# Performance work log

Measured on AMD Instinct MI355X. Metric: run time of the kernel, lower is better.

## Reference

```python
import jax, jax.numpy as jnp
import numpy as np

N = 100000  # nodes
E = 1600000  # edges (before self-loops)
F_IN, F_HID, F_OUT = 64, 128, 64


def setup_inputs() -> dict:
    key = jax.random.key(0)
    ks = jax.random.split(key, 8)
    x = jax.random.normal(ks[0], (N, F_IN), dtype=jnp.float32)
    edge_index = jax.random.randint(ks[1], (2, E), 0, N, dtype=jnp.int64)
    # Glorot-ish init for weights, zero bias (PyG GCNConv default)
    W1 = jax.random.normal(ks[2], (F_IN, F_HID), dtype=jnp.float32) / np.sqrt(F_IN)
    W2 = jax.random.normal(ks[3], (F_HID, F_HID), dtype=jnp.float32) / np.sqrt(F_HID)
    W3 = jax.random.normal(ks[4], (F_HID, F_OUT), dtype=jnp.float32) / np.sqrt(F_HID)
    b1 = jnp.zeros((F_HID,), dtype=jnp.float32)
    b2 = jnp.zeros((F_HID,), dtype=jnp.float32)
    b3 = jnp.zeros((F_OUT,), dtype=jnp.float32)
    return {"x": x, "edge_index": edge_index, "W1": W1, "b1": b1,
            "W2": W2, "b2": b2, "W3": W3, "b3": b3}


def _gcn_norm(edge_index, num_nodes):
    """Add self-loops and compute symmetric D^-1/2 A D^-1/2 edge norms."""
    loop = jnp.arange(num_nodes, dtype=edge_index.dtype)
    src = jnp.concatenate([edge_index[0], loop])  # [E+N]
    dst = jnp.concatenate([edge_index[1], loop])  # [E+N]
    deg = jax.ops.segment_sum(jnp.ones_like(src, dtype=jnp.float32), dst,
                              num_segments=num_nodes)
    dinv = jnp.where(deg > 0, jax.lax.rsqrt(deg), 0.0)
    norm = dinv[src] * dinv[dst]  # [E+N]
    return src, dst, norm


def _gcn_conv(h, src, dst, norm, W, b, num_nodes):
    hw = h @ W                                   # [N, out] dense transform
    msg = hw[src] * norm[:, None]                # gather + edge scale
    out = jax.ops.segment_sum(msg, dst, num_segments=num_nodes)  # scatter-add
    return out + b


def reference(x, edge_index, W1, b1, W2, b2, W3, b3):
    src, dst, norm = _gcn_norm(edge_index, N)
    h = jax.nn.relu(_gcn_conv(x, src, dst, norm, W1, b1, N))
    h = jax.nn.relu(_gcn_conv(h, src, dst, norm, W2, b2, N))
    return _gcn_conv(h, src, dst, norm, W3, b3, N)
```

## Files before the change

### kernel.cpp

```cpp
#include <hip/hip_runtime.h>
#include <hip/hip_bf16.h>
#include <hip/hip_fp16.h>


typedef _Float16 h8 __attribute__((ext_vector_type(8)));
typedef float f4 __attribute__((ext_vector_type(4)));

constexpr int BSHIFT = 7;
constexpr int BNODES = 1 << BSHIFT;
constexpr int PB     = 256;
constexpr int CAP    = 4096;

__device__ inline void load8h(const _Float16* p, float* f) {
    h8 v = *(const h8*)p;
#pragma unroll
    for (int j = 0; j < 8; j++) f[j] = (float)v[j];
}

__device__ inline void store8h(_Float16* p, const float* f) {
    h8 v;
#pragma unroll
    for (int j = 0; j < 8; j++) v[j] = (_Float16)f[j];
    *(h8*)p = v;
}

__device__ inline void store4h(_Float16* p, float4 v) {
    _Float16 t[4] = {(_Float16)v.x, (_Float16)v.y, (_Float16)v.z, (_Float16)v.w};
    *(uint2*)p = *(uint2*)t;
}

__global__ __launch_bounds__(256) void phist_k(const int* __restrict__ dst,
                                               int* __restrict__ hist,
                                               int E, int nbuck, int chunk) {
    __shared__ int h[1024];
    for (int i = threadIdx.x; i < nbuck; i += 256) h[i] = 0;
    __syncthreads();
    int beg = blockIdx.x * chunk;
    int end = min(E, beg + chunk);
    for (int e = beg + threadIdx.x; e < end; e += 256)
        atomicAdd(&h[dst[e] >> BSHIFT], 1);
    __syncthreads();
    for (int i = threadIdx.x; i < nbuck; i += 256)
        hist[(long)blockIdx.x * nbuck + i] = h[i];
}

__global__ __launch_bounds__(256) void scan_blocks_k(const int* __restrict__ in,
                                                     int* __restrict__ excl,
                                                     int* __restrict__ bsums, int n) {
    __shared__ int s[256];
    int tid = threadIdx.x;
    int i = blockIdx.x * 256 + tid;
    int v = (i < n) ? in[i] : 0;
    s[tid] = v;
    __syncthreads();
    for (int off = 1; off < 256; off <<= 1) {
        int t = (tid >= off) ? s[tid - off] : 0;
        __syncthreads();
        s[tid] += t;
        __syncthreads();
    }
    if (i < n) excl[i] = s[tid] - v;
    if (tid == 255) bsums[blockIdx.x] = s[255];
}

__global__ __launch_bounds__(1024) void mid_k(int* __restrict__ bsums, int nb,
                                              const int* __restrict__ hist,
                                              int* __restrict__ bbase,
                                              int nbuck, int E) {
    __shared__ int s[1024];
    int tid = threadIdx.x;
    int v = 0;
    if (blockIdx.x == 0) {
        v = (tid < nb) ? bsums[tid] : 0;
    } else {
        if (tid < nbuck) {
            int t0 = 0, t1 = 0, t2 = 0, t3 = 0;
            for (int j = 0; j < PB; j += 4) {
                t0 += hist[(long)(j + 0) * nbuck + tid];
                t1 += hist[(long)(j + 1) * nbuck + tid];
                t2 += hist[(long)(j + 2) * nbuck + tid];
                t3 += hist[(long)(j + 3) * nbuck + tid];
            }
            v = (t0 + t1) + (t2 + t3);
        }
    }
    s[tid] = v;
    __syncthreads();
    for (int off = 1; off < 1024; off <<= 1) {
        int t = (tid >= off) ? s[tid - off] : 0;
        __syncthreads();
        s[tid] += t;
        __syncthreads();
    }
    if (blockIdx.x == 0) {
        if (tid < nb) bsums[tid] = s[tid] - v;
    } else {
        if (tid < nbuck) bbase[tid] = s[tid] - v;
        if (tid == 0) bbase[nbuck] = E;
    }
}

__global__ __launch_bounds__(256) void part2_k(const int* __restrict__ src,
                                               const int* __restrict__ dst,
                                               const int* __restrict__ offs,
                                               const int* __restrict__ bsums,
                                               unsigned* __restrict__ ebuf,
                                               int E, int nbuck, int chunk) {
    __shared__ int cur[1024];
    for (int i = threadIdx.x; i < nbuck; i += 256) {
        long flat = (long)blockIdx.x * nbuck + i;
        cur[i] = offs[flat] + bsums[flat >> 8];
    }
    __syncthreads();
    int beg = blockIdx.x * chunk;
    int end = min(E, beg + chunk);
    for (int e = beg + threadIdx.x; e < end; e += 256) {
        int d = dst[e];
        int b = d >> BSHIFT;
        int pos = atomicAdd(&cur[b], 1);
        ebuf[pos] = ((unsigned)(d & (BNODES - 1)) << 25) | (unsigned)src[e];
    }
}

__global__ __launch_bounds__(256) void finalize_k(const unsigned* __restrict__ ebuf,
                                                  const int* __restrict__ hist,
                                                  const int* __restrict__ offs,
                                                  const int* __restrict__ bsums,
                                                  const int* __restrict__ bbase,
                                                  int nbuck,
                                                  int* __restrict__ rowst,
                                                  int* __restrict__ rowend,
                                                  float* __restrict__ dinv,
                                                  int* __restrict__ col,
                                                  const float* __restrict__ x,
                                                  _Float16* __restrict__ msgX, int N) {
    __shared__ unsigned se[CAP];
    __shared__ int cj[PB], sj[PB], sb[PB];
    __shared__ int cnt_s[BNODES], scan_s[BNODES], cur_s[BNODES];
    __shared__ float di_s[BNODES];

    int b = blockIdx.x, tid = threadIdx.x;
    int node0 = b << BSHIFT;
    int nn = min(BNODES, N - node0);
    int beg = bbase[b];

    if (tid < PB) {
        long flat = (long)tid * nbuck + b;
        cj[tid] = hist[flat];
        sj[tid] = offs[flat] + bsums[flat >> 8];
    }
    if (tid < BNODES) cnt_s[tid] = 0;
    __syncthreads();

    if (tid < PB) sb[tid] = cj[tid];
    __syncthreads();
    for (int off = 1; off < PB; off <<= 1) {
        int t = 0;
        if (tid < PB && tid >= off) t = sb[tid - off];
        __syncthreads();
        if (tid < PB) sb[tid] += t;
        __syncthreads();
    }
    int m = sb[PB - 1];
    __syncthreads();

    {
        int j = tid;
        int base = sb[j] - cj[j], c = cj[j], s0 = sj[j];
        for (int k = 0; k < c; k++) {
            unsigned e = ebuf[s0 + k];
            int idx = base + k;
            if (idx < CAP) se[idx] = e;
            else atomicAdd(&cnt_s[e >> 25], 1);
        }
    }
    __syncthreads();

    int mcap = m < CAP ? m : CAP;
    for (int i = tid; i < mcap; i += 256) atomicAdd(&cnt_s[se[i] >> 25], 1);
    __syncthreads();

    int v = (tid < BNODES) ? cnt_s[tid] : 0;
    if (tid < BNODES) scan_s[tid] = v;
    __syncthreads();
    for (int off = 1; off < BNODES; off <<= 1) {
        int t = 0;
        if (tid < BNODES && tid >= off) t = scan_s[tid - off];
        __syncthreads();
        if (tid < BNODES) scan_s[tid] += t;
        __syncthreads();
    }
    if (tid < nn) {
        int ex = scan_s[tid] - v;
        int st = beg + ex;
        rowst[node0 + tid] = st;
        rowend[node0 + tid] = st + v;
        float di = rsqrtf((float)v + 1.0f);
        dinv[node0 + tid] = di;
        di_s[tid] = di;
        cur_s[tid] = ex;
    }
    __syncthreads();

    for (int i = tid; i < mcap; i += 256) {
        unsigned e = se[i];
        int p = atomicAdd(&cur_s[e >> 25], 1);
        col[beg + p] = (int)(e & 0x1FFFFFFu);
    }
    if (m > CAP) {
        int j = tid;
        int base = sb[j] - cj[j], c = cj[j], s0 = sj[j];
        for (int k = 0; k < c; k++) {
            int idx = base + k;
            if (idx >= CAP) {
                unsigned e = ebuf[s0 + k];
                int p = atomicAdd(&cur_s[e >> 25], 1);
                col[beg + p] = (int)(e & 0x1FFFFFFu);
            }
        }
    }

    for (int t = tid; t < nn * 16; t += 256) {
        int nl = t >> 4, q = t & 15;
        int node = node0 + nl;
        float4 vx = *(const float4*)(x + (long)node * 64 + q * 4);
        float di = di_s[nl];
        vx.x *= di; vx.y *= di; vx.z *= di; vx.w *= di;
        store4h(msgX + (long)node * 64 + q * 4, vx);
    }
}

template <int K, int FOUT, bool BIAS, bool RELU, bool DINV_OUT, bool SMOUT>
__global__ __launch_bounds__(256) void fag_k(const _Float16* __restrict__ msg,
                                             const int* __restrict__ rowst,
                                             const int* __restrict__ rowend,
                                             const int* __restrict__ col,
                                             const float* __restrict__ dinv,
                                             const _Float16* __restrict__ Wsw,
                                             const float* __restrict__ bias,
                                             _Float16* __restrict__ C, int n) {
    constexpr int NT = FOUT / 16, NC = K / 32;
    constexpr int LDK = K + 8;
    constexpr int LPN = K / 8;
    constexpr int NPB = 256 / LPN;
    __shared__ _Float16 As[64 * LDK];

    int tid = threadIdx.x;
    int row0 = blockIdx.x * 64;

#pragma unroll
    for (int pass = 0; pass < 64 / NPB; pass++) {
        int nl = pass * NPB + tid / LPN;
        int q = tid % LPN;
        int node = row0 + nl;
        float acc[8];
        if (node < n) {
            load8h(msg + (long)node * K + q * 8, acc);
            int beg = rowst[node], end = rowend[node];
            int e = beg;
            for (; e + 4 <= end; e += 4) {
                int s0 = col[e], s1 = col[e + 1], s2 = col[e + 2], s3 = col[e + 3];
                h8 v0 = *(const h8*)(msg + (long)s0 * K + q * 8);
                h8 v1 = *(const h8*)(msg + (long)s1 * K + q * 8);
                h8 v2 = *(const h8*)(msg + (long)s2 * K + q * 8);
                h8 v3 = *(const h8*)(msg + (long)s3 * K + q * 8);
#pragma unroll
                for (int j = 0; j < 8; j++)
                    acc[j] += ((float)v0[j] + (float)v1[j]) + ((float)v2[j] + (float)v3[j]);
            }
            for (; e < end; e++) {
                int s = col[e];
                h8 v = *(const h8*)(msg + (long)s * K + q * 8);
#pragma unroll
                for (int j = 0; j < 8; j++) acc[j] += (float)v[j];
            }
            float di = dinv[node];
#pragma unroll
            for (int j = 0; j < 8; j++) acc[j] *= di;
        } else {
#pragma unroll
            for (int j = 0; j < 8; j++) acc[j] = 0.f;
        }
        h8 o;
#pragma unroll
        for (int j = 0; j < 8; j++) o[j] = (_Float16)acc[j];
        *(h8*)(As + nl * LDK + q * 8) = o;
    }
    __syncthreads();

    int lane = tid & 63, wave = tid >> 6;
    int quad = lane >> 4, cl = lane & 15;
    int r0 = wave * 16;

    h8 a[NC];
#pragma unroll
    for (int c = 0; c < NC; c++)
        a[c] = *(const h8*)(As + (r0 + cl) * LDK + quad * 8 + c * 32);

    f4 acc2[NT];
#pragma unroll
    for (int t = 0; t < NT; t++) acc2[t] = (f4){0.f, 0.f, 0.f, 0.f};

    const h8* wv = (const h8*)Wsw;
#pragma unroll
    for (int c = 0; c < NC; c++) {
#pragma unroll
        for (int t = 0; t < NT; t++)
            acc2[t] = __builtin_amdgcn_mfma_f32_16x16x32_f16(
                a[c], wv[(c * NT + t) * 64 + lane], acc2[t], 0, 0, 0);
    }

#pragma unroll
    for (int t = 0; t < NT; t++) {
        int c0 = t * 16 + cl;
        float bb = BIAS ? bias[c0] : 0.f;
#pragma unroll
        for (int r = 0; r < 4; r++) {
            int row = row0 + r0 + quad * 4 + r;
            if (row >= n) continue;
            float v = acc2[t][r] + bb;
            if (RELU) v = fmaxf(v, 0.f);
            if (DINV_OUT) v *= dinv[row];
            if (SMOUT)
                C[((long)t * n + row) * 16 + cl] = (_Float16)v;
            else
                C[(long)row * FOUT + c0] = (_Float16)v;
        }
    }
}

__global__ __launch_bounds__(256) void agg_sm2_k(const _Float16* __restrict__ msg,
                                                 const int* __restrict__ rowst,
                                                 const int* __restrict__ rowend,
                                                 const int* __restrict__ col,
                                                 const float* __restrict__ dinv,
                                                 _Float16* __restrict__ out, int n) {
    int slice = blockIdx.x & 7;
    int blk   = blockIdx.x >> 3;
    int node  = blk * 128 + (threadIdx.x >> 1);
    int q     = threadIdx.x & 1;
    if (node >= n) return;
    const _Float16* mp = msg + (long)slice * n * 16 + q * 8;

    float acc[8];
    load8h(mp + (long)node * 16, acc);

    int beg = rowst[node], end = rowend[node];
    int e = beg;
    for (; e + 8 <= end; e += 8) {
        h8 v[8];
#pragma unroll
        for (int u = 0; u < 8; u++)
            v[u] = *(const h8*)(mp + (long)col[e + u] * 16);
#pragma unroll
        for (int j = 0; j < 8; j++)
            acc[j] += (((float)v[0][j] + (float)v[1][j]) + ((float)v[2][j] + (float)v[3][j])) +
                      (((float)v[4][j] + (float)v[5][j]) + ((float)v[6][j] + (float)v[7][j]));
    }
    for (; e + 4 <= end; e += 4) {
        h8 v0 = *(const h8*)(mp + (long)col[e] * 16);
        h8 v1 = *(const h8*)(mp + (long)col[e + 1] * 16);
        h8 v2 = *(const h8*)(mp + (long)col[e + 2] * 16);
        h8 v3 = *(const h8*)(mp + (long)col[e + 3] * 16);
#pragma unroll
        for (int j = 0; j < 8; j++)
            acc[j] += ((float)v0[j] + (float)v1[j]) + ((float)v2[j] + (float)v3[j]);
    }
    for (; e < end; e++) {
        h8 v = *(const h8*)(mp + (long)col[e] * 16);
#pragma unroll
        for (int j = 0; j < 8; j++) acc[j] += (float)v[j];
    }

    float di = dinv[node];
    float o[8];
#pragma unroll
    for (int j = 0; j < 8; j++) o[j] = di * acc[j];
    store8h(out + (long)node * 128 + slice * 16 + q * 8, o);
}

__global__ __launch_bounds__(256) void agg_sm3_k(const _Float16* __restrict__ msg,
                                                 const int* __restrict__ rowst,
                                                 const int* __restrict__ rowend,
                                                 const int* __restrict__ col,
                                                 const float* __restrict__ dinv,
                                                 const float* __restrict__ b,
                                                 float* __restrict__ out, int n) {
    int slice = blockIdx.x & 7;
    int blk   = blockIdx.x >> 3;
    int node  = blk * 256 + threadIdx.x;
    if (node >= n) return;
    const _Float16* mp = msg + (long)slice * n * 8;

    float acc[8];
    load8h(mp + (long)node * 8, acc);

    int beg = rowst[node], end = rowend[node];
    int e = beg;
    for (; e + 8 <= end; e += 8) {
        h8 v[8];
#pragma unroll
        for (int u = 0; u < 8; u++)
            v[u] = *(const h8*)(mp + (long)col[e + u] * 8);
#pragma unroll
        for (int j = 0; j < 8; j++)
            acc[j] += (((float)v[0][j] + (float)v[1][j]) + ((float)v[2][j] + (float)v[3][j])) +
                      (((float)v[4][j] + (float)v[5][j]) + ((float)v[6][j] + (float)v[7][j]));
    }
    for (; e + 4 <= end; e += 4) {
        h8 v0 = *(const h8*)(mp + (long)col[e] * 8);
        h8 v1 = *(const h8*)(mp + (long)col[e + 1] * 8);
        h8 v2 = *(const h8*)(mp + (long)col[e + 2] * 8);
        h8 v3 = *(const h8*)(mp + (long)col[e + 3] * 8);
#pragma unroll
        for (int j = 0; j < 8; j++)
            acc[j] += ((float)v0[j] + (float)v1[j]) + ((float)v2[j] + (float)v3[j]);
    }
    for (; e < end; e++) {
        h8 v = *(const h8*)(mp + (long)col[e] * 8);
#pragma unroll
        for (int j = 0; j < 8; j++) acc[j] += (float)v[j];
    }

    float di = dinv[node];
    float o[8];
#pragma unroll
    for (int j = 0; j < 8; j++) o[j] = di * acc[j] + b[slice * 8 + j];
    float* d = out + (long)node * 64 + slice * 8;
    *(float4*)d = make_float4(o[0], o[1], o[2], o[3]);
    *(float4*)(d + 4) = make_float4(o[4], o[5], o[6], o[7]);
}

template <int K, int FOUT>
__device__ inline void wfrag(const float* __restrict__ W,
                             _Float16* __restrict__ Wsw, int t) {
    constexpr int NT = FOUT / 16;
    int lane = t & 63;
    int tile = (t >> 6) % NT;
    int chunk = (t >> 6) / NT;
    int kbase = chunk * 32 + (lane >> 4) * 8;
    int nc = tile * 16 + (lane & 15);
    h8 v;
#pragma unroll
    for (int j = 0; j < 8; j++) v[j] = (_Float16)W[(kbase + j) * FOUT + nc];
    ((h8*)Wsw)[t] = v;
}

__global__ __launch_bounds__(256) void wprep3_k(const float* __restrict__ W1,
                                                const float* __restrict__ W2,
                                                const float* __restrict__ W3,
                                                _Float16* __restrict__ w1s,
                                                _Float16* __restrict__ w2s,
                                                _Float16* __restrict__ w3s) {
    int t = blockIdx.x * 256 + threadIdx.x;
    if (t < 1024) wfrag<64, 128>(W1, w1s, t);
    else if (t < 3072) wfrag<128, 128>(W2, w2s, t - 1024);
    else if (t < 4096) wfrag<128, 64>(W3, w3s, t - 3072);
}

__global__ __launch_bounds__(256) void dgemm_k(const _Float16* __restrict__ A,
                                               const _Float16* __restrict__ w2s,
                                               const _Float16* __restrict__ w3s,
                                               const float* __restrict__ b2,
                                               const float* __restrict__ dinv,
                                               _Float16* __restrict__ C, int n) {
    constexpr int LDK = 136;
    __shared__ _Float16 Hs[64 * LDK];

    int tid = threadIdx.x, lane = tid & 63, wave = tid >> 6;
    int quad = lane >> 4, cl = lane & 15;
    int row0 = blockIdx.x * 64, r0 = wave * 16;

    h8 a[4];
    const _Float16* arow = A + (long)(row0 + r0 + cl) * 128 + quad * 8;
#pragma unroll
    for (int c = 0; c < 4; c++) a[c] = *(const h8*)(arow + c * 32);

    f4 acc1[8];
#pragma unroll
    for (int t = 0; t < 8; t++) acc1[t] = (f4){0.f, 0.f, 0.f, 0.f};
    const h8* wv2 = (const h8*)w2s;
#pragma unroll
    for (int c = 0; c < 4; c++) {
#pragma unroll
        for (int t = 0; t < 8; t++)
            acc1[t] = __builtin_amdgcn_mfma_f32_16x16x32_f16(
                a[c], wv2[(c * 8 + t) * 64 + lane], acc1[t], 0, 0, 0);
    }

#pragma unroll
    for (int t = 0; t < 8; t++) {
        int c0 = t * 16 + cl;
        float bb = b2[c0];
#pragma unroll
        for (int r = 0; r < 4; r++) {
            float v = fmaxf(acc1[t][r] + bb, 0.f);
            Hs[(r0 + quad * 4 + r) * LDK + c0] = (_Float16)v;
        }
    }
    __builtin_amdgcn_s_waitcnt(0);

    h8 a2[4];
#pragma unroll
    for (int c = 0; c < 4; c++)
        a2[c] = *(const h8*)(Hs + (r0 + cl) * LDK + quad * 8 + c * 32);

    f4 acc2[4];
#pragma unroll
    for (int t = 0; t < 4; t++) acc2[t] = (f4){0.f, 0.f, 0.f, 0.f};
    const h8* wv3 = (const h8*)w3s;
#pragma unroll
    for (int c = 0; c < 4; c++) {
#pragma unroll
        for (int t = 0; t < 4; t++)
            acc2[t] = __builtin_amdgcn_mfma_f32_16x16x32_f16(
                a2[c], wv3[(c * 4 + t) * 64 + lane], acc2[t], 0, 0, 0);
    }

#pragma unroll
    for (int t = 0; t < 4; t++) {
        int c0 = t * 16 + cl;
        int sl = c0 >> 3, sp = c0 & 7;
#pragma unroll
        for (int r = 0; r < 4; r++) {
            int row = row0 + r0 + quad * 4 + r;
            if (row >= n) continue;
            float v = acc2[t][r] * dinv[row];
            C[((long)sl * n + row) * 8 + sp] = (_Float16)v;
        }
    }
}

extern "C" void kernel_launch(void* const* d_in, const int* in_sizes, int n_in,
                              void* d_out, int out_size, void* d_ws, size_t ws_size,
                              hipStream_t stream) {
    const float* x  = (const float*)d_in[0];
    const int*   ei = (const int*)d_in[1];
    const float* W1 = (const float*)d_in[2];
    const float* b1 = (const float*)d_in[3];
    const float* W2 = (const float*)d_in[4];
    const float* b2 = (const float*)d_in[5];
    const float* W3 = (const float*)d_in[6];
    const float* b3 = (const float*)d_in[7];
    float* out = (float*)d_out;

    const int N = in_sizes[0] / 64;
    const int E = in_sizes[1] / 2;
    const int* src = ei;
    const int* dst = ei + E;
    const int nbuck = (N + BNODES - 1) >> BSHIFT;
    const int chunk = (E + PB - 1) / PB;
    const int n2 = PB * nbuck;
    const int nb2 = (n2 + 255) / 256;

    int*   hist   = (int*)d_ws;
    int*   offs   = hist + n2;
    int*   bsums  = offs + n2;
    int*   bbase  = bsums + 1024;
    int*   rowst  = bbase + nbuck + 1;
    int*   rowend = rowst + N;
    float* dinv   = (float*)(rowend + N);
    int*   col    = (int*)(dinv + N);
    _Float16* w1s = (_Float16*)(col + E);
    _Float16* w2s = w1s + 64 * 128;
    _Float16* w3s = w2s + 128 * 128;
    float* P      = (float*)(w3s + 128 * 64);
    float* Q      = P + (long)N * 128;

    _Float16* msgX  = (_Float16*)P;
    unsigned* ebuf  = (unsigned*)Q;
    _Float16* msg1  = (_Float16*)Q;
    _Float16* aggH1 = (_Float16*)P;
    _Float16* msg3  = (_Float16*)Q;

    const int gb = (N + 63) / 64;

    wprep3_k<<<16, 256, 0, stream>>>(W1, W2, W3, w1s, w2s, w3s);

    phist_k<<<PB, 256, 0, stream>>>(dst, hist, E, nbuck, chunk);
    scan_blocks_k<<<nb2, 256, 0, stream>>>(hist, offs, bsums, n2);
    mid_k<<<2, 1024, 0, stream>>>(bsums, nb2, hist, bbase, nbuck, E);
    part2_k<<<PB, 256, 0, stream>>>(src, dst, offs, bsums, ebuf, E, nbuck, chunk);
    finalize_k<<<nbuck, 256, 0, stream>>>(ebuf, hist, offs, bsums, bbase, nbuck,
                                          rowst, rowend, dinv, col, x, msgX, N);

    fag_k<64, 128, true, true, true, true><<<gb, 256, 0, stream>>>(
        msgX, rowst, rowend, col, dinv, w1s, b1, msg1, N);

    const int nb128 = (N + 127) / 128;
    agg_sm2_k<<<8 * nb128, 256, 0, stream>>>(
        msg1, rowst, rowend, col, dinv, aggH1, N);

    dgemm_k<<<gb, 256, 0, stream>>>(aggH1, w2s, w3s, b2, dinv, msg3, N);

    const int nb256 = (N + 255) / 256;
    agg_sm3_k<<<8 * nb256, 256, 0, stream>>>(
        msg3, rowst, rowend, col, dinv, b3, out, N);
}
```

Measured before the change: 433.3 us.

## Split each node's edge list across 8 lanes with shuffle reduction in aggregation

Both aggregation kernels now give each node 8 threads, which take edges in an interleaved stride and combine partial sums with xor-shuffles, instead of one or two threads walking the whole edge list. The layer-2 aggregation output is also written slice-major, and the dense GEMM reads its A operand from that layout so each store is contiguous. The aim is more memory-level parallelism per node and less load imbalance from skewed degrees. The cost is more threads per node, shuffle overhead, and a loss of long per-thread unrolled gather chains.

```diff
diff --git a/kernel.cpp b/kernel.cpp
--- a/kernel.cpp
+++ b/kernel.cpp
@@ -329,7 +329,7 @@
     }
 }
 
-__global__ __launch_bounds__(256) void agg_sm2_k(const _Float16* __restrict__ msg,
+__global__ __launch_bounds__(256) void agg_ep2_k(const _Float16* __restrict__ msg,
                                                  const int* __restrict__ rowst,
                                                  const int* __restrict__ rowend,
                                                  const int* __restrict__ col,
@@ -337,49 +337,53 @@
                                                  _Float16* __restrict__ out, int n) {
     int slice = blockIdx.x & 7;
     int blk   = blockIdx.x >> 3;
-    int node  = blk * 128 + (threadIdx.x >> 1);
-    int q     = threadIdx.x & 1;
+    int tid   = threadIdx.x;
+    int node  = blk * 32 + (tid >> 3);
+    int eslot = (tid >> 1) & 3;
+    int q     = tid & 1;
     if (node >= n) return;
     const _Float16* mp = msg + (long)slice * n * 16 + q * 8;
 
     float acc[8];
-    load8h(mp + (long)node * 16, acc);
+    if (eslot == 0) {
+        load8h(mp + (long)node * 16, acc);
+    } else {
+#pragma unroll
+        for (int j = 0; j < 8; j++) acc[j] = 0.f;
+    }
 
     int beg = rowst[node], end = rowend[node];
-    int e = beg;
-    for (; e + 8 <= end; e += 8) {
-        h8 v[8];
-#pragma unroll
-        for (int u = 0; u < 8; u++)
-            v[u] = *(const h8*)(mp + (long)col[e + u] * 16);
-#pragma unroll
-        for (int j = 0; j < 8; j++)
-            acc[j] += (((float)v[0][j] + (float)v[1][j]) + ((float)v[2][j] + (float)v[3][j])) +
-                      (((float)v[4][j] + (float)v[5][j]) + ((float)v[6][j] + (float)v[7][j]));
-    }
-    for (; e + 4 <= end; e += 4) {
-        h8 v0 = *(const h8*)(mp + (long)col[e] * 16);
-        h8 v1 = *(const h8*)(mp + (long)col[e + 1] * 16);
-        h8 v2 = *(const h8*)(mp + (long)col[e + 2] * 16);
-        h8 v3 = *(const h8*)(mp + (long)col[e + 3] * 16);
-#pragma unroll
-        for (int j = 0; j < 8; j++)
-            acc[j] += ((float)v0[j] + (float)v1[j]) + ((float)v2[j] + (float)v3[j]);
-    }
-    for (; e < end; e++) {
-        h8 v = *(const h8*)(mp + (long)col[e] * 16);
+    int e = beg + eslot;
+    for (; e + 4 < end; e += 8) {
+        int s0 = col[e], s1 = col[e + 4];
+        h8 v0 = *(const h8*)(mp + (long)s0 * 16);
+        h8 v1 = *(const h8*)(mp + (long)s1 * 16);
+#pragma unroll
+        for (int j = 0; j < 8; j++) acc[j] += (float)v0[j] + (float)v1[j];
+    }
+    if (e < end) {
+        int s = col[e];
+        h8 v = *(const h8*)(mp + (long)s * 16);
 #pragma unroll
         for (int j = 0; j < 8; j++) acc[j] += (float)v[j];
     }
 
-    float di = dinv[node];
-    float o[8];
-#pragma unroll
-    for (int j = 0; j < 8; j++) o[j] = di * acc[j];
-    store8h(out + (long)node * 128 + slice * 16 + q * 8, o);
-}
-
-__global__ __launch_bounds__(256) void agg_sm3_k(const _Float16* __restrict__ msg,
+#pragma unroll
+    for (int j = 0; j < 8; j++) {
+        acc[j] += __shfl_xor(acc[j], 2);
+        acc[j] += __shfl_xor(acc[j], 4);
+    }
+
+    if ((tid & 6) == 0) {
+        float di = dinv[node];
+        float o[8];
+#pragma unroll
+        for (int j = 0; j < 8; j++) o[j] = di * acc[j];
+        store8h(out + ((long)slice * n + node) * 16 + q * 8, o);
+    }
+}
+
+__global__ __launch_bounds__(256) void agg_ep3_k(const _Float16* __restrict__ msg,
                                                  const int* __restrict__ rowst,
                                                  const int* __restrict__ rowend,
                                                  const int* __restrict__ col,
@@ -388,47 +392,52 @@
                                                  float* __restrict__ out, int n) {
     int slice = blockIdx.x & 7;
     int blk   = blockIdx.x >> 3;
-    int node  = blk * 256 + threadIdx.x;
+    int tid   = threadIdx.x;
+    int node  = blk * 32 + (tid >> 3);
+    int eslot = tid & 7;
     if (node >= n) return;
     const _Float16* mp = msg + (long)slice * n * 8;
 
     float acc[8];
-    load8h(mp + (long)node * 8, acc);
+    if (eslot == 0) {
+        load8h(mp + (long)node * 8, acc);
+    } else {
+#pragma unroll
+        for (int j = 0; j < 8; j++) acc[j] = 0.f;
+    }
 
     int beg = rowst[node], end = rowend[node];
-    int e = beg;
-    for (; e + 8 <= end; e += 8) {
-        h8 v[8];
-#pragma unroll
-        for (int u = 0; u < 8; u++)
-            v[u] = *(const h8*)(mp + (long)col[e + u] * 8);
-#pragma unroll
-        for (int j = 0; j < 8; j++)
-            acc[j] += (((float)v[0][j] + (float)v[1][j]) + ((float)v[2][j] + (float)v[3][j])) +
-                      (((float)v[4][j] + (float)v[5][j]) + ((float)v[6][j] + (float)v[7][j]));
-    }
-    for (; e + 4 <= end; e += 4) {
-        h8 v0 = *(const h8*)(mp + (long)col[e] * 8);
-        h8 v1 = *(const h8*)(mp + (long)col[e + 1] * 8);
-        h8 v2 = *(const h8*)(mp + (long)col[e + 2] * 8);
-        h8 v3 = *(const h8*)(mp + (long)col[e + 3] * 8);
-#pragma unroll
-        for (int j = 0; j < 8; j++)
-            acc[j] += ((float)v0[j] + (float)v1[j]) + ((float)v2[j] + (float)v3[j]);
-    }
-    for (; e < end; e++) {
-        h8 v = *(const h8*)(mp + (long)col[e] * 8);
+    int e = beg + eslot;
+    for (; e + 8 < end; e += 16) {
+        int s0 = col[e], s1 = col[e + 8];
+        h8 v0 = *(const h8*)(mp + (long)s0 * 8);
+        h8 v1 = *(const h8*)(mp + (long)s1 * 8);
+#pragma unroll
+        for (int j = 0; j < 8; j++) acc[j] += (float)v0[j] + (float)v1[j];
+    }
+    if (e < end) {
+        int s = col[e];
+        h8 v = *(const h8*)(mp + (long)s * 8);
 #pragma unroll
         for (int j = 0; j < 8; j++) acc[j] += (float)v[j];
     }
 
-    float di = dinv[node];
-    float o[8];
-#pragma unroll
-    for (int j = 0; j < 8; j++) o[j] = di * acc[j] + b[slice * 8 + j];
-    float* d = out + (long)node * 64 + slice * 8;
-    *(float4*)d = make_float4(o[0], o[1], o[2], o[3]);
-    *(float4*)(d + 4) = make_float4(o[4], o[5], o[6], o[7]);
+#pragma unroll
+    for (int j = 0; j < 8; j++) {
+        acc[j] += __shfl_xor(acc[j], 1);
+        acc[j] += __shfl_xor(acc[j], 2);
+        acc[j] += __shfl_xor(acc[j], 4);
+    }
+
+    if (eslot == 0) {
+        float di = dinv[node];
+        float o[8];
+#pragma unroll
+        for (int j = 0; j < 8; j++) o[j] = di * acc[j] + b[slice * 8 + j];
+        float* d = out + (long)node * 64 + slice * 8;
+        *(float4*)d = make_float4(o[0], o[1], o[2], o[3]);
+        *(float4*)(d + 4) = make_float4(o[4], o[5], o[6], o[7]);
+    }
 }
 
 template <int K, int FOUT>
@@ -470,11 +479,14 @@
     int tid = threadIdx.x, lane = tid & 63, wave = tid >> 6;
     int quad = lane >> 4, cl = lane & 15;
     int row0 = blockIdx.x * 64, r0 = wave * 16;
+    int arow = row0 + r0 + cl;
 
     h8 a[4];
-    const _Float16* arow = A + (long)(row0 + r0 + cl) * 128 + quad * 8;
-#pragma unroll
-    for (int c = 0; c < 4; c++) a[c] = *(const h8*)(arow + c * 32);
+#pragma unroll
+    for (int c = 0; c < 4; c++) {
+        int sl = c * 2 + (quad >> 1);
+        a[c] = *(const h8*)(A + ((long)sl * n + arow) * 16 + (quad & 1) * 8);
+    }
 
     f4 acc1[8];
 #pragma unroll
@@ -570,7 +582,7 @@
     _Float16* msgX  = (_Float16*)P;
     unsigned* ebuf  = (unsigned*)Q;
     _Float16* msg1  = (_Float16*)Q;
-    _Float16* aggH1 = (_Float16*)P;
+    _Float16* aggH2 = (_Float16*)P;
     _Float16* msg3  = (_Float16*)Q;
 
     const int gb = (N + 63) / 64;
@@ -587,13 +599,12 @@
     fag_k<64, 128, true, true, true, true><<<gb, 256, 0, stream>>>(
         msgX, rowst, rowend, col, dinv, w1s, b1, msg1, N);
 
-    const int nb128 = (N + 127) / 128;
-    agg_sm2_k<<<8 * nb128, 256, 0, stream>>>(
-        msg1, rowst, rowend, col, dinv, aggH1, N);
-
-    dgemm_k<<<gb, 256, 0, stream>>>(aggH1, w2s, w3s, b2, dinv, msg3, N);
-
-    const int nb256 = (N + 255) / 256;
-    agg_sm3_k<<<8 * nb256, 256, 0, stream>>>(
+    const int nb32 = (N + 31) / 32;
+    agg_ep2_k<<<8 * nb32, 256, 0, stream>>>(
+        msg1, rowst, rowend, col, dinv, aggH2, N);
+
+    dgemm_k<<<gb, 256, 0, stream>>>(aggH2, w2s, w3s, b2, dinv, msg3, N);
+
+    agg_ep3_k<<<8 * nb32, 256, 0, stream>>>(
         msg3, rowst, rowend, col, dinv, b3, out, N);
 }
```

New measurement: 402.9 us. 7.0% less time.
